# Kernel optimization log

Measured on AMD Instinct MI355X. Metric: run time of the kernel, lower is better.

## Reference

```python
import jax, jax.numpy as jnp
import numpy as np

N = 100000       # nodes
E = 1000000      # edges
IN = 128         # in_dim
HID = 64         # hid_dim
NET = 4          # n_etypes
STEPS = 5        # n_steps
G = 128          # graphs in batch
LBL = 10         # num_labels


def setup_inputs() -> dict:
    key = jax.random.key(0)
    ks = jax.random.split(key, 20)
    def w(k, shape, fan_in):
        return jax.random.normal(k, shape, jnp.float32) / np.sqrt(fan_in)
    return dict(
        x=jax.random.normal(ks[0], (N, IN), jnp.float32),
        src=jax.random.randint(ks[1], (E,), 0, N),
        dst=jax.random.randint(ks[2], (E,), 0, N),
        etype=jax.random.randint(ks[3], (E,), 0, NET),
        node2graph=jnp.sort(jax.random.randint(ks[4], (N,), 0, G)),
        # linear_in
        W_in=w(ks[5], (HID, IN), IN), b_in=jnp.zeros((HID,), jnp.float32),
        # per-edge-type linears [n_etypes, out, in]
        We=w(ks[6], (NET, HID, HID), HID), be=jnp.zeros((NET, HID), jnp.float32),
        # GRUCell (torch layout: rows = [r; z; n])
        W_ih=w(ks[7], (3 * HID, HID), HID), b_ih=jnp.zeros((3 * HID,), jnp.float32),
        W_hh=w(ks[8], (3 * HID, HID), HID), b_hh=jnp.zeros((3 * HID,), jnp.float32),
        # classifier
        W1=w(ks[9], (HID // 2, HID), HID), b1=jnp.zeros((HID // 2,), jnp.float32),
        W2=w(ks[10], (LBL, HID // 2), HID // 2), b2=jnp.zeros((LBL,), jnp.float32),
    )


def reference(x, W_in, b_in, We, be, W_ih, b_ih, W_hh, b_hh, W1, b1, W2, b2,
              src, dst, etype, node2graph):
    h = x @ W_in.T + b_in                                  # [N, HID]
    for _ in range(STEPS):
        # per-etype linear on node states: trans[e] = h @ We[e].T + be[e]
        trans = jnp.einsum('nd,efd->enf', h, We) + be[:, None, :]  # [NET, N, HID]
        msgs = trans[etype, src]                           # [E, HID] gather per edge
        a = jax.ops.segment_sum(msgs, dst, num_segments=N)  # scatter-add aggregation
        # GRUCell(a, h)
        gi = a @ W_ih.T + b_ih
        gh = h @ W_hh.T + b_hh
        ir, iz, i_n = jnp.split(gi, 3, axis=-1)
        hr, hz, h_n = jnp.split(gh, 3, axis=-1)
        r = jax.nn.sigmoid(ir + hr)
        z = jax.nn.sigmoid(iz + hz)
        n = jnp.tanh(i_n + r * h_n)
        h = (1.0 - z) * n + z * h
    # dgl.mean_nodes: per-graph mean of node states
    cnt = jnp.maximum(jax.ops.segment_sum(jnp.ones((N,), h.dtype), node2graph, num_segments=G), 1.0)
    hg = jax.ops.segment_sum(h, node2graph, num_segments=G) / cnt[:, None]  # [G, HID]
    return jax.nn.relu(hg @ W1.T + b1) @ W2.T + b2         # [G, LBL]
```

## Files before the change

kernel.cpp:

```cpp
#include <hip/hip_runtime.h>
#include <hip/hip_bf16.h>
#include <math.h>

#define N_NODES 100000
#define N_EDGES 1000000
#define IN_DIM 128
#define HID 64
#define NET 4
#define STEPS 5
#define G_GRAPHS 128
#define LBL 10
#define NGRP 6250
#define NBKT 1024
#define TILE_E 8192

typedef __attribute__((ext_vector_type(8))) short short8;
typedef __attribute__((ext_vector_type(4))) float f32x4;
typedef unsigned short ushort_t;

__device__ inline ushort_t f2bf(float v) {
    __hip_bfloat16 b = __float2bfloat16(v);
    return __builtin_bit_cast(ushort_t, b);
}
__device__ inline float bf2f(ushort_t u) {
    __hip_bfloat16 b = __builtin_bit_cast(__hip_bfloat16, u);
    return __bfloat162float(b);
}


__global__ void k_pack_bc(const float* __restrict__ We, ushort_t* __restrict__ BC) {
    int idx = blockIdx.x * blockDim.x + threadIdx.x;
    if (idx >= 24 * 4 * 64 * 8) return;
    int j = idx & 7, lane = (idx >> 3) & 63, ct = (idx >> 9) & 3, sl = idx >> 11;
    int g = lane >> 4, u = lane & 15;
    int p = sl >> 3, ks = sl & 7;
    int k = ks * 32 + g * 8 + j;
    int t = k >> 6, d = k & 63;
    int o = ct * 16 + u;
    float val = We[t * 4096 + o * 64 + d];
    ushort_t hi = f2bf(val);
    BC[idx] = (p < 2) ? hi : f2bf(val - bf2f(hi));
}

__global__ void k_pack_b2(const float* __restrict__ W_ih, const float* __restrict__ b_ih,
                          const float* __restrict__ W_hh, const float* __restrict__ b_hh,
                          ushort_t* __restrict__ B2, float* __restrict__ bg2) {
    int idx = blockIdx.x * blockDim.x + threadIdx.x;
    if (idx >= 12 * 16 * 4 * 16 * 8) return;
    int j = idx & 7, u = (idx >> 3) & 15, g = (idx >> 7) & 3, ct = (idx >> 9) & 15, s = idx >> 13;
    int m = ct * 16 + u;
    int q = m >> 6, gate = (m >> 4) & 3, c = q * 16 + (m & 15);
    int k = (s & 3) * 32 + g * 8 + j;
    float val;
    if (gate == 0)      { int jr = c;        val = (k < 64) ? W_ih[jr * 64 + k] : W_hh[jr * 64 + k - 64]; }
    else if (gate == 1) { int jr = 64 + c;   val = (k < 64) ? W_ih[jr * 64 + k] : W_hh[jr * 64 + k - 64]; }
    else if (gate == 2) { int jr = 128 + c;  val = (k < 64) ? W_ih[jr * 64 + k] : 0.f; }
    else                { int jr = 128 + c;  val = (k < 64) ? 0.f : W_hh[jr * 64 + k - 64]; }
    ushort_t hi = f2bf(val);
    B2[idx] = (s < 8) ? hi : f2bf(val - bf2f(hi));
    if (s == 0 && g == 0 && j == 0) {
        float bv;
        if (gate == 0)      bv = b_ih[c] + b_hh[c];
        else if (gate == 1) bv = b_ih[64 + c] + b_hh[64 + c];
        else if (gate == 2) bv = b_ih[128 + c];
        else                bv = b_hh[128 + c];
        bg2[m] = bv;
    }
}

__global__ void k_pack_bin(const float* __restrict__ W_in, ushort_t* __restrict__ BIN) {
    int idx = blockIdx.x * blockDim.x + threadIdx.x;
    if (idx >= 24576) return;
    int j = idx & 7, lu = (idx >> 3) & 63, ct = (idx >> 9) & 3, s = idx >> 11;
    int g = lu >> 4, u = lu & 15;
    int m = ct * 16 + u;
    int k = (s & 3) * 32 + g * 8 + j;
    float val = W_in[m * 128 + k];
    ushort_t hi = f2bf(val);
    BIN[idx] = (s < 8) ? hi : f2bf(val - bf2f(hi));
}

__global__ __launch_bounds__(256) void k_linear_in(const float* __restrict__ x,
        const ushort_t* __restrict__ BIN, const float* __restrict__ b_in,
        ushort_t* __restrict__ hrow, ushort_t* __restrict__ lrow) {
    __shared__ float hlds[4][16 * 68];
    int tid = threadIdx.x;
    int lane = tid & 63, wp = tid >> 6;
    int g = lane >> 4, u = lane & 15;
    int grp = blockIdx.x * 4 + wp;
    bool ok = grp < NGRP;
    int row = ok ? (grp * 16 + u) : 0;
    short8 xhi[4], xlo[4];
    #pragma unroll
    for (int ks = 0; ks < 4; ++ks) {
        const float* xp = &x[(size_t)row * 128 + ks * 32 + g * 8];
        float4 v0 = ok ? *(const float4*)xp : make_float4(0.f, 0.f, 0.f, 0.f);
        float4 v1 = ok ? *(const float4*)(xp + 4) : make_float4(0.f, 0.f, 0.f, 0.f);
        float vv[8] = {v0.x, v0.y, v0.z, v0.w, v1.x, v1.y, v1.z, v1.w};
        #pragma unroll
        for (int j = 0; j < 8; ++j) {
            ushort_t hh = f2bf(vv[j]);
            xhi[ks][j] = (short)hh;
            xlo[ks][j] = (short)f2bf(vv[j] - bf2f(hh));
        }
    }
    f32x4 zero = {0.f, 0.f, 0.f, 0.f};
    f32x4 acc[4] = {zero, zero, zero, zero};
    #pragma unroll
    for (int s = 0; s < 12; ++s) {
        int ks = s & 3;
        short8 af = (s < 4) ? xhi[ks] : (s < 8) ? xlo[ks] : xhi[ks];
        #pragma unroll
        for (int ct = 0; ct < 4; ++ct) {
            short8 bf = *(const short8*)&BIN[((size_t)(s * 4 + ct) * 64 + lane) * 8];
            acc[ct] = __builtin_amdgcn_mfma_f32_16x16x32_bf16(af, bf, acc[ct], 0, 0, 0);
        }
    }
    #pragma unroll
    for (int ct = 0; ct < 4; ++ct) {
        float bo = b_in[ct * 16 + u];
        #pragma unroll
        for (int j = 0; j < 4; ++j)
            hlds[wp][(g * 4 + j) * 68 + ct * 16 + u] = acc[ct][j] + bo;
    }
    __syncthreads();
    #pragma unroll
    for (int k = 0; k < 4; ++k) {
        int bi = g + 4 * k;
        short8 ov;
        #pragma unroll
        for (int j = 0; j < 8; ++j) {
            float v = hlds[wp][u * 68 + (bi & 7) * 8 + j];
            ushort_t hh = f2bf(v);
            ov[j] = (bi < 8) ? (short)hh : (short)f2bf(v - bf2f(hh));
        }
        if (ok) {
            size_t base = (size_t)(grp * 16 + u) * 64;
            if (bi < 8) *(short8*)&hrow[base + bi * 8] = ov;
            else        *(short8*)&lrow[base + (bi - 8) * 8] = ov;
        }
    }
}

__global__ __launch_bounds__(256) void k_bhist(const int* __restrict__ dst,
        int* __restrict__ bhist) {
    __shared__ int h[NBKT];
    for (int i = threadIdx.x; i < NBKT; i += 256) h[i] = 0;
    __syncthreads();
    int idx = blockIdx.x * 256 + threadIdx.x;
    for (int e = idx; e < N_EDGES; e += 256 * 256) atomicAdd(&h[dst[e] >> 7], 1);
    __syncthreads();
    for (int i = threadIdx.x; i < NBKT; i += 256) {
        int c = h[i];
        if (c) atomicAdd(&bhist[i], c);
    }
}

__global__ __launch_bounds__(1024) void k_bscan(const int* __restrict__ bhist,
        int* __restrict__ bbase, int* __restrict__ bcursor) {
    __shared__ int ts[NBKT];
    int t = threadIdx.x;
    int v = bhist[t];
    ts[t] = v;
    __syncthreads();
    for (int off = 1; off < NBKT; off <<= 1) {
        int u = (t >= off) ? ts[t - off] : 0;
        __syncthreads();
        ts[t] += u;
        __syncthreads();
    }
    int excl = ts[t] - v;
    bbase[t] = excl;
    bcursor[t] = excl;
    if (t == NBKT - 1) bbase[NBKT] = ts[NBKT - 1];
}

__global__ __launch_bounds__(512) void k_bscatter(const int* __restrict__ src,
        const int* __restrict__ dst, const int* __restrict__ et,
        int* __restrict__ bcursor, unsigned int* __restrict__ ebuf) {
    __shared__ int hcnt[NBKT], loff[NBKT], gpos[NBKT], ps[512];
    __shared__ unsigned int stage[TILE_E];
    __shared__ unsigned short sbkt[TILE_E];
    int tid = threadIdx.x;
    int base = blockIdx.x * TILE_E;
    int tilecnt = min(TILE_E, N_EDGES - base);
    for (int i = tid; i < NBKT; i += 512) hcnt[i] = 0;
    __syncthreads();
    #pragma unroll
    for (int k = 0; k < TILE_E / 512; ++k) {
        int e = base + tid + k * 512;
        if (e < N_EDGES) atomicAdd(&hcnt[dst[e] >> 7], 1);
    }
    __syncthreads();
    int c0 = hcnt[tid * 2], c1 = hcnt[tid * 2 + 1];
    ps[tid] = c0 + c1;
    __syncthreads();
    for (int off = 1; off < 512; off <<= 1) {
        int u = (tid >= off) ? ps[tid - off] : 0;
        __syncthreads();
        ps[tid] += u;
        __syncthreads();
    }
    int ex = ps[tid] - (c0 + c1);
    loff[tid * 2] = ex;
    loff[tid * 2 + 1] = ex + c0;
    for (int b = tid; b < NBKT; b += 512) {
        int c = hcnt[b];
        gpos[b] = c ? atomicAdd(&bcursor[b], c) : 0;
    }
    __syncthreads();
    for (int i = tid; i < NBKT; i += 512) hcnt[i] = 0;
    __syncthreads();
    #pragma unroll
    for (int k = 0; k < TILE_E / 512; ++k) {
        int e = base + tid + k * 512;
        if (e < N_EDGES) {
            int d = dst[e];
            int b = d >> 7;
            int r = atomicAdd(&hcnt[b], 1);
            int lp = loff[b] + r;
            stage[lp] = (unsigned int)src[e] | ((unsigned int)et[e] << 20)
                      | ((unsigned int)(d & 127) << 22);
            sbkt[lp] = (unsigned short)b;
        }
    }
    __syncthreads();
    for (int i = tid; i < tilecnt; i += 512) {
        int b = sbkt[i];
        ebuf[gpos[b] + (i - loff[b])] = stage[i];
    }
}

__global__ __launch_bounds__(256) void k_bcsr(const unsigned int* __restrict__ ebuf,
        const int* __restrict__ bbase, int* __restrict__ adj, int* __restrict__ row_ptr2) {
    __shared__ int ncnt[512], noff[513], ps[256];
    int b = blockIdx.x;
    int tid = threadIdx.x;
    int ebeg = bbase[b], eend = bbase[b + 1];
    int ecnt = eend - ebeg;
    ncnt[tid] = 0; ncnt[tid + 256] = 0;
    __syncthreads();
    for (int i = tid; i < ecnt; i += 256) {
        unsigned int p = ebuf[ebeg + i];
        int key = (int)((((p >> 22) & 127) << 2) | ((p >> 20) & 3));
        atomicAdd(&ncnt[key], 1);
    }
    __syncthreads();
    int c0 = ncnt[2 * tid], c1 = ncnt[2 * tid + 1];
    ps[tid] = c0 + c1;
    __syncthreads();
    for (int off = 1; off < 256; off <<= 1) {
        int u = (tid >= off) ? ps[tid - off] : 0;
        __syncthreads();
        ps[tid] += u;
        __syncthreads();
    }
    int ex = ps[tid] - (c0 + c1);
    noff[2 * tid] = ex;
    noff[2 * tid + 1] = ex + c0;
    if (tid == 255) noff[512] = ps[255];
    __syncthreads();
    ncnt[tid] = 0; ncnt[tid + 256] = 0;
    __syncthreads();
    for (int i = tid; i < ecnt; i += 256) {
        unsigned int p = ebuf[ebeg + i];
        int key = (int)((((p >> 22) & 127) << 2) | ((p >> 20) & 3));
        int r = atomicAdd(&ncnt[key], 1);
        adj[ebeg + noff[key] + r] = (int)(p & 0xFFFFF);
    }
    for (int k = tid; k < 512; k += 256)
        row_ptr2[b * 512 + k] = ebeg + noff[k];
    if (b == NBKT - 1 && tid == 0) row_ptr2[NBKT * 512] = eend;
}

__global__ __launch_bounds__(512) void k_step(const int* __restrict__ row_ptr2,
        const int* __restrict__ adj, const ushort_t* __restrict__ hin,
        const ushort_t* __restrict__ lin, ushort_t* __restrict__ hout,
        ushort_t* __restrict__ lout,
        const ushort_t* __restrict__ BC, const float* __restrict__ be,
        const ushort_t* __restrict__ B2, const float* __restrict__ bg2) {
    __shared__ float smem[8448];
    float* aggf = smem;
    float* cnts = smem + 8320;
    ushort_t* als  = (ushort_t*)smem;
    ushort_t* hlds = (ushort_t*)((char*)smem + 9216);

    int tid = threadIdx.x, lane = tid & 63, wp = tid >> 6;
    int g = lane >> 4, u = lane & 15;
    int grp0 = blockIdx.x * 2;
    int nbase = grp0 * 16;

    #pragma unroll 1
    for (int pr = 0; pr < 2; ++pr) {
        int nl0 = wp * 4 + pr * 2;
        const int* op = &row_ptr2[(size_t)(nbase + nl0) * 4];
        int b0 = op[0], b1 = op[1], b2 = op[2], b3 = op[3], b4 = op[4];
        int b5 = op[5], b6 = op[6], b7 = op[7], b8 = op[8];
        int i0 = b0, i1 = b1, i2 = b2, i3 = b3, i4 = b4, i5 = b5, i6 = b6, i7 = b7;
        float s0 = 0.f, s1 = 0.f, s2 = 0.f, s3 = 0.f, s4 = 0.f, s5 = 0.f, s6 = 0.f, s7 = 0.f;
        bool c0 = i0 < b1, c1 = i1 < b2, c2 = i2 < b3, c3 = i3 < b4;
        bool c4 = i4 < b5, c5 = i5 < b6, c6 = i6 < b7, c7 = i7 < b8;
        int a0 = adj[c0 ? i0 : 0], a1 = adj[c1 ? i1 : 0];
        int a2 = adj[c2 ? i2 : 0], a3 = adj[c3 ? i3 : 0];
        int a4 = adj[c4 ? i4 : 0], a5 = adj[c5 ? i5 : 0];
        int a6 = adj[c6 ? i6 : 0], a7 = adj[c7 ? i7 : 0];
        while (c0 | c1 | c2 | c3 | c4 | c5 | c6 | c7) {
            ushort_t w0 = hin[(size_t)a0 * 64 + lane];
            ushort_t w1 = hin[(size_t)a1 * 64 + lane];
            ushort_t w2 = hin[(size_t)a2 * 64 + lane];
            ushort_t w3 = hin[(size_t)a3 * 64 + lane];
            ushort_t w4 = hin[(size_t)a4 * 64 + lane];
            ushort_t w5 = hin[(size_t)a5 * 64 + lane];
            ushort_t w6 = hin[(size_t)a6 * 64 + lane];
            ushort_t w7 = hin[(size_t)a7 * 64 + lane];
            i0 += c0; i1 += c1; i2 += c2; i3 += c3;
            i4 += c4; i5 += c5; i6 += c6; i7 += c7;
            s0 += c0 ? bf2f(w0) : 0.f;
            s1 += c1 ? bf2f(w1) : 0.f;
            s2 += c2 ? bf2f(w2) : 0.f;
            s3 += c3 ? bf2f(w3) : 0.f;
            s4 += c4 ? bf2f(w4) : 0.f;
            s5 += c5 ? bf2f(w5) : 0.f;
            s6 += c6 ? bf2f(w6) : 0.f;
            s7 += c7 ? bf2f(w7) : 0.f;
            c0 = i0 < b1; c1 = i1 < b2; c2 = i2 < b3; c3 = i3 < b4;
            c4 = i4 < b5; c5 = i5 < b6; c6 = i6 < b7; c7 = i7 < b8;
            a0 = adj[c0 ? i0 : 0]; a1 = adj[c1 ? i1 : 0];
            a2 = adj[c2 ? i2 : 0]; a3 = adj[c3 ? i3 : 0];
            a4 = adj[c4 ? i4 : 0]; a5 = adj[c5 ? i5 : 0];
            a6 = adj[c6 ? i6 : 0]; a7 = adj[c7 ? i7 : 0];
        }
        aggf[nl0 * 260 +   0 + lane] = s0;
        aggf[nl0 * 260 +  64 + lane] = s1;
        aggf[nl0 * 260 + 128 + lane] = s2;
        aggf[nl0 * 260 + 192 + lane] = s3;
        aggf[(nl0 + 1) * 260 +   0 + lane] = s4;
        aggf[(nl0 + 1) * 260 +  64 + lane] = s5;
        aggf[(nl0 + 1) * 260 + 128 + lane] = s6;
        aggf[(nl0 + 1) * 260 + 192 + lane] = s7;
        if (lane == 0) {
            cnts[nl0 * 4 + 0] = (float)(b1 - b0);
            cnts[nl0 * 4 + 1] = (float)(b2 - b1);
            cnts[nl0 * 4 + 2] = (float)(b3 - b2);
            cnts[nl0 * 4 + 3] = (float)(b4 - b3);
            cnts[(nl0 + 1) * 4 + 0] = (float)(b5 - b4);
            cnts[(nl0 + 1) * 4 + 1] = (float)(b6 - b5);
            cnts[(nl0 + 1) * 4 + 2] = (float)(b7 - b6);
            cnts[(nl0 + 1) * 4 + 3] = (float)(b8 - b7);
        }
    }
    __syncthreads();

    int rp1 = wp >> 2, cq = wp & 3;
    f32x4 zero = {0.f, 0.f, 0.f, 0.f};
    f32x4 acc1 = zero;
    #pragma unroll
    for (int ks = 0; ks < 8; ++ks) {
        const float* ap = &aggf[(rp1 * 16 + u) * 260 + ks * 32 + g * 8];
        f32x4 x0 = *(const f32x4*)ap;
        f32x4 x1 = *(const f32x4*)(ap + 4);
        short8 ahi, alo;
        #pragma unroll
        for (int j = 0; j < 4; ++j) {
            ushort_t hh = f2bf(x0[j]);
            ahi[j] = (short)hh; alo[j] = (short)f2bf(x0[j] - bf2f(hh));
            ushort_t hh2 = f2bf(x1[j]);
            ahi[4 + j] = (short)hh2; alo[4 + j] = (short)f2bf(x1[j] - bf2f(hh2));
        }
        #pragma unroll
        for (int p = 0; p < 3; ++p) {
            short8 af = (p == 1) ? alo : ahi;
            short8 bf = *(const short8*)&BC[((size_t)((p * 8 + ks) * 4 + cq) * 64 + lane) * 8];
            acc1 = __builtin_amdgcn_mfma_f32_16x16x32_bf16(af, bf, acc1, 0, 0, 0);
        }
    }
    __syncthreads();

    {
        float beL[4];
        #pragma unroll
        for (int t = 0; t < 4; ++t) beL[t] = be[t * 64 + cq * 16 + u];
        #pragma unroll
        for (int j = 0; j < 4; ++j) {
            int row = rp1 * 16 + g * 4 + j;
            f32x4 cn = *(const f32x4*)&cnts[row * 4];
            float v = acc1[j] + cn[0] * beL[0] + cn[1] * beL[1]
                              + cn[2] * beL[2] + cn[3] * beL[3];
            int col = cq * 16 + u;
            ushort_t hh = f2bf(v);
            als[row * 136 + col] = hh;
            als[row * 136 + 64 + col] = f2bf(v - bf2f(hh));
        }
    }
    {
        int c = tid;
        int gl = c >> 8, rr = c & 255, bi = rr >> 4, uu = rr & 15;
        size_t base = (size_t)(nbase + gl * 16 + uu) * 64;
        short8 v = (bi < 8) ? *(const short8*)&hin[base + bi * 8]
                            : *(const short8*)&lin[base + (bi - 8) * 8];
        *(short8*)&hlds[((gl * 16 + bi) * 16 + uu) * 8] = v;
    }
    __syncthreads();

    int q = wp & 3, rp2 = wp >> 2;
    f32x4 acc2[4] = {zero, zero, zero, zero};
    #pragma unroll
    for (int s = 0; s < 12; ++s) {
        int p2 = s >> 2, ks2 = s & 3;
        short8 afr;
        if (ks2 < 2) {
            int base = ((p2 == 1) ? 64 : 0) + ks2 * 32 + g * 8;
            afr = *(const short8*)&als[(rp2 * 16 + u) * 136 + base];
        } else {
            int part = (p2 == 1) ? 1 : 0;
            int bi = part * 8 + (ks2 - 2) * 4 + g;
            afr = *(const short8*)&hlds[((rp2 * 16 + bi) * 16 + u) * 8];
        }
        #pragma unroll
        for (int ct = 0; ct < 4; ++ct) {
            short8 bfr = *(const short8*)&B2[((size_t)(s * 16 + q * 4 + ct) * 64 + g * 16 + u) * 8];
            acc2[ct] = __builtin_amdgcn_mfma_f32_16x16x32_bf16(afr, bfr, acc2[ct], 0, 0, 0);
        }
    }
    __syncthreads();

    {
        float bgv[4];
        #pragma unroll
        for (int ct = 0; ct < 4; ++ct) bgv[ct] = bg2[q * 64 + ct * 16 + u];
        int hid = q * 16 + u;
        #pragma unroll
        for (int j = 0; j < 4; ++j) {
            int uu = g * 4 + j;
            int shi = ((rp2 * 16 + (hid >> 3)) * 16 + uu) * 8 + (hid & 7);
            int slo = ((rp2 * 16 + 8 + (hid >> 3)) * 16 + uu) * 8 + (hid & 7);
            float ho = bf2f(hlds[shi]) + bf2f(hlds[slo]);
            float rs  = acc2[0][j] + bgv[0];
            float zs  = acc2[1][j] + bgv[1];
            float inn = acc2[2][j] + bgv[2];
            float hnn = acc2[3][j] + bgv[3];
            float rr = 1.f / (1.f + __expf(-rs));
            float zz = 1.f / (1.f + __expf(-zs));
            float t = inn + rr * hnn;
            float e2 = __expf(2.f * t);
            float nn = 1.f - 2.f / (e2 + 1.f);
            float hnew = (1.f - zz) * nn + zz * ho;
            ushort_t hh = f2bf(hnew);
            hlds[shi] = hh;
            hlds[slo] = f2bf(hnew - bf2f(hh));
        }
    }
    __syncthreads();

    {
        int c = tid;
        int gl = c >> 8, rr = c & 255, bi = rr >> 4, uu = rr & 15;
        short8 v = *(const short8*)&hlds[((gl * 16 + bi) * 16 + uu) * 8];
        size_t base = (size_t)(nbase + gl * 16 + uu) * 64;
        if (bi < 8) *(short8*)&hout[base + bi * 8] = v;
        else        *(short8*)&lout[base + (bi - 8) * 8] = v;
    }
}

__global__ __launch_bounds__(256) void k_pool(const int* __restrict__ n2g,
        const ushort_t* __restrict__ hrow, const ushort_t* __restrict__ lrow,
        float* __restrict__ hg) {
    int gidx = blockIdx.x;
    int lo = 0, hi = N_NODES;
    while (lo < hi) { int mid = (lo + hi) >> 1; if (n2g[mid] < gidx) lo = mid + 1; else hi = mid; }
    int s = lo;
    hi = N_NODES;
    while (lo < hi) { int mid = (lo + hi) >> 1; if (n2g[mid] < gidx + 1) lo = mid + 1; else hi = mid; }
    int e = lo;
    int w = threadIdx.x >> 6, lane = threadIdx.x & 63;
    float sum = 0.f;
    for (int n = s + w; n < e; n += 4)
        sum += bf2f(hrow[(size_t)n * 64 + lane]) + bf2f(lrow[(size_t)n * 64 + lane]);
    __shared__ float red[4][64];
    red[w][lane] = sum;
    __syncthreads();
    if (threadIdx.x < 64) {
        float tot = red[0][lane] + red[1][lane] + red[2][lane] + red[3][lane];
        float cnt = (float)(e - s);
        hg[gidx * 64 + lane] = tot / fmaxf(cnt, 1.f);
    }
}

__global__ __launch_bounds__(64) void k_cls(const float* __restrict__ hg,
        const float* __restrict__ W1, const float* __restrict__ b1,
        const float* __restrict__ W2, const float* __restrict__ b2,
        float* __restrict__ out) {
    int gidx = blockIdx.x;
    __shared__ float v[64];
    __shared__ float m[32];
    v[threadIdx.x] = hg[gidx * 64 + threadIdx.x];
    __syncthreads();
    if (threadIdx.x < 32) {
        float a = b1[threadIdx.x];
        #pragma unroll 8
        for (int k = 0; k < 64; ++k) a = fmaf(v[k], W1[threadIdx.x * 64 + k], a);
        m[threadIdx.x] = fmaxf(a, 0.f);
    }
    __syncthreads();
    if (threadIdx.x < 10) {
        float a = b2[threadIdx.x];
        #pragma unroll
        for (int j = 0; j < 32; ++j) a = fmaf(m[j], W2[threadIdx.x * 32 + j], a);
        out[gidx * 10 + threadIdx.x] = a;
    }
}

extern "C" void kernel_launch(void* const* d_in, const int* in_sizes, int n_in,
                              void* d_out, int out_size, void* d_ws, size_t ws_size,
                              hipStream_t stream) {
    const float* x    = (const float*)d_in[0];
    const int* src    = (const int*)d_in[1];
    const int* dst    = (const int*)d_in[2];
    const int* etype  = (const int*)d_in[3];
    const int* n2g    = (const int*)d_in[4];
    const float* W_in = (const float*)d_in[5];
    const float* b_in = (const float*)d_in[6];
    const float* We   = (const float*)d_in[7];
    const float* be   = (const float*)d_in[8];
    const float* W_ih = (const float*)d_in[9];
    const float* b_ih = (const float*)d_in[10];
    const float* W_hh = (const float*)d_in[11];
    const float* b_hh = (const float*)d_in[12];
    const float* W1   = (const float*)d_in[13];
    const float* b1   = (const float*)d_in[14];
    const float* W2   = (const float*)d_in[15];
    const float* b2   = (const float*)d_in[16];
    float* out = (float*)d_out;

    char* wsb = (char*)d_ws;
    size_t off = 0;
    auto alloc = [&](size_t bytes) -> void* {
        void* p = wsb + off;
        off += (bytes + 255) & ~(size_t)255;
        return p;
    };
    ushort_t* hrowA    = (ushort_t*)alloc((size_t)N_NODES * 64 * 2);
    ushort_t* lrowA    = (ushort_t*)alloc((size_t)N_NODES * 64 * 2);
    ushort_t* hrowB    = (ushort_t*)alloc((size_t)N_NODES * 64 * 2);
    ushort_t* lrowB    = (ushort_t*)alloc((size_t)N_NODES * 64 * 2);
    int*      adj      = (int*)     alloc((size_t)N_EDGES * 4);
    unsigned int* ebuf = (unsigned int*)alloc((size_t)N_EDGES * 4);
    int*      row_ptr2 = (int*)     alloc(((size_t)NBKT * 512 + 1) * 4);
    int*      bhist    = (int*)     alloc((size_t)NBKT * 4);
    int*      bbase    = (int*)     alloc((size_t)(NBKT + 1) * 4);
    int*      bcursor  = (int*)     alloc((size_t)NBKT * 4);
    ushort_t* B2       = (ushort_t*)alloc((size_t)12 * 16 * 4 * 16 * 8 * 2);
    float*    bg2      = (float*)   alloc(256 * 4);
    ushort_t* BIN      = (ushort_t*)alloc((size_t)24576 * 2);
    ushort_t* BC       = (ushort_t*)alloc((size_t)24 * 4 * 64 * 8 * 2);
    float*    hg       = (float*)   alloc(128 * 64 * 4);

    hipLaunchKernelGGL(k_pack_b2, dim3(384), dim3(256), 0, stream, W_ih, b_ih, W_hh, b_hh, B2, bg2);
    hipLaunchKernelGGL(k_pack_bin, dim3(96), dim3(256), 0, stream, W_in, BIN);
    hipLaunchKernelGGL(k_pack_bc, dim3(192), dim3(256), 0, stream, We, BC);
    hipLaunchKernelGGL(k_linear_in, dim3((NGRP + 3) / 4), dim3(256), 0, stream, x, BIN, b_in, hrowA, lrowA);

    hipMemsetAsync(bhist, 0, (size_t)NBKT * 4, stream);
    hipLaunchKernelGGL(k_bhist, dim3(256), dim3(256), 0, stream, dst, bhist);
    hipLaunchKernelGGL(k_bscan, dim3(1), dim3(1024), 0, stream, bhist, bbase, bcursor);
    hipLaunchKernelGGL(k_bscatter, dim3((N_EDGES + TILE_E - 1) / TILE_E), dim3(512), 0, stream,
                       src, dst, etype, bcursor, ebuf);
    hipLaunchKernelGGL(k_bcsr, dim3(NBKT), dim3(256), 0, stream, ebuf, bbase, adj, row_ptr2);

    int sblk = NGRP / 2;
    for (int step = 0; step < STEPS; ++step) {
        const ushort_t* hin = (step & 1) ? hrowB : hrowA;
        const ushort_t* lin = (step & 1) ? lrowB : lrowA;
        ushort_t* hout      = (step & 1) ? hrowA : hrowB;
        ushort_t* lout      = (step & 1) ? lrowA : lrowB;
        hipLaunchKernelGGL(k_step, dim3(sblk), dim3(512), 0, stream,
                           row_ptr2, adj, hin, lin, hout, lout, BC, be, B2, bg2);
    }
    hipLaunchKernelGGL(k_pool, dim3(G_GRAPHS), dim3(256), 0, stream, n2g, hrowB, lrowB, hg);
    hipLaunchKernelGGL(k_cls, dim3(G_GRAPHS), dim3(64), 0, stream, hg, W1, b1, W2, b2, out);
}
```

Baseline: 816.7 us.

## Balance per-block edge aggregation across waves with LDS atomics; truncate bf16 splits

The per-node, per-etype segmented gather loop is replaced. Each wave now takes an equal slice of the block's contiguous edge range and accumulates into LDS with float atomics, using node and etype bits packed into the adjacency word. This targets load imbalance and the idle lanes of the old eight-way predicated loop, at the cost of LDS atomic contention and an extra zeroing pass. Separately, the bf16 hi/lo splits now use bit truncation instead of round-to-nearest conversion, which saves some ALU work and keeps the hi+lo split accurate.

```diff
diff --git a/kernel.cpp b/kernel.cpp
--- a/kernel.cpp
+++ b/kernel.cpp
@@ -232,7 +232,8 @@
 }
 
 __global__ __launch_bounds__(256) void k_bcsr(const unsigned int* __restrict__ ebuf,
-        const int* __restrict__ bbase, int* __restrict__ adj, int* __restrict__ row_ptr2) {
+        const int* __restrict__ bbase, unsigned int* __restrict__ adj,
+        int* __restrict__ row_ptr2) {
     __shared__ int ncnt[512], noff[513], ps[256];
     int b = blockIdx.x;
     int tid = threadIdx.x;
@@ -266,7 +267,7 @@
         unsigned int p = ebuf[ebeg + i];
         int key = (int)((((p >> 22) & 127) << 2) | ((p >> 20) & 3));
         int r = atomicAdd(&ncnt[key], 1);
-        adj[ebeg + noff[key] + r] = (int)(p & 0xFFFFF);
+        adj[ebeg + noff[key] + r] = p & 0x07FFFFFFu;
     }
     for (int k = tid; k < 512; k += 256)
         row_ptr2[b * 512 + k] = ebeg + noff[k];
@@ -274,14 +275,14 @@
 }
 
 __global__ __launch_bounds__(512) void k_step(const int* __restrict__ row_ptr2,
-        const int* __restrict__ adj, const ushort_t* __restrict__ hin,
+        const unsigned int* __restrict__ adj, const ushort_t* __restrict__ hin,
         const ushort_t* __restrict__ lin, ushort_t* __restrict__ hout,
         ushort_t* __restrict__ lout,
         const ushort_t* __restrict__ BC, const float* __restrict__ be,
         const ushort_t* __restrict__ B2, const float* __restrict__ bg2) {
     __shared__ float smem[8448];
+    __shared__ int rp[129];
     float* aggf = smem;
-    float* cnts = smem + 8320;
     ushort_t* als  = (ushort_t*)smem;
     ushort_t* hlds = (ushort_t*)((char*)smem + 9216);
 
@@ -290,63 +291,44 @@
     int grp0 = blockIdx.x * 2;
     int nbase = grp0 * 16;
 
-    #pragma unroll 1
-    for (int pr = 0; pr < 2; ++pr) {
-        int nl0 = wp * 4 + pr * 2;
-        const int* op = &row_ptr2[(size_t)(nbase + nl0) * 4];
-        int b0 = op[0], b1 = op[1], b2 = op[2], b3 = op[3], b4 = op[4];
-        int b5 = op[5], b6 = op[6], b7 = op[7], b8 = op[8];
-        int i0 = b0, i1 = b1, i2 = b2, i3 = b3, i4 = b4, i5 = b5, i6 = b6, i7 = b7;
-        float s0 = 0.f, s1 = 0.f, s2 = 0.f, s3 = 0.f, s4 = 0.f, s5 = 0.f, s6 = 0.f, s7 = 0.f;
-        bool c0 = i0 < b1, c1 = i1 < b2, c2 = i2 < b3, c3 = i3 < b4;
-        bool c4 = i4 < b5, c5 = i5 < b6, c6 = i6 < b7, c7 = i7 < b8;
-        int a0 = adj[c0 ? i0 : 0], a1 = adj[c1 ? i1 : 0];
-        int a2 = adj[c2 ? i2 : 0], a3 = adj[c3 ? i3 : 0];
-        int a4 = adj[c4 ? i4 : 0], a5 = adj[c5 ? i5 : 0];
-        int a6 = adj[c6 ? i6 : 0], a7 = adj[c7 ? i7 : 0];
-        while (c0 | c1 | c2 | c3 | c4 | c5 | c6 | c7) {
-            ushort_t w0 = hin[(size_t)a0 * 64 + lane];
-            ushort_t w1 = hin[(size_t)a1 * 64 + lane];
-            ushort_t w2 = hin[(size_t)a2 * 64 + lane];
-            ushort_t w3 = hin[(size_t)a3 * 64 + lane];
-            ushort_t w4 = hin[(size_t)a4 * 64 + lane];
-            ushort_t w5 = hin[(size_t)a5 * 64 + lane];
-            ushort_t w6 = hin[(size_t)a6 * 64 + lane];
-            ushort_t w7 = hin[(size_t)a7 * 64 + lane];
-            i0 += c0; i1 += c1; i2 += c2; i3 += c3;
-            i4 += c4; i5 += c5; i6 += c6; i7 += c7;
-            s0 += c0 ? bf2f(w0) : 0.f;
-            s1 += c1 ? bf2f(w1) : 0.f;
-            s2 += c2 ? bf2f(w2) : 0.f;
-            s3 += c3 ? bf2f(w3) : 0.f;
-            s4 += c4 ? bf2f(w4) : 0.f;
-            s5 += c5 ? bf2f(w5) : 0.f;
-            s6 += c6 ? bf2f(w6) : 0.f;
-            s7 += c7 ? bf2f(w7) : 0.f;
-            c0 = i0 < b1; c1 = i1 < b2; c2 = i2 < b3; c3 = i3 < b4;
-            c4 = i4 < b5; c5 = i5 < b6; c6 = i6 < b7; c7 = i7 < b8;
-            a0 = adj[c0 ? i0 : 0]; a1 = adj[c1 ? i1 : 0];
-            a2 = adj[c2 ? i2 : 0]; a3 = adj[c3 ? i3 : 0];
-            a4 = adj[c4 ? i4 : 0]; a5 = adj[c5 ? i5 : 0];
-            a6 = adj[c6 ? i6 : 0]; a7 = adj[c7 ? i7 : 0];
-        }
-        aggf[nl0 * 260 +   0 + lane] = s0;
-        aggf[nl0 * 260 +  64 + lane] = s1;
-        aggf[nl0 * 260 + 128 + lane] = s2;
-        aggf[nl0 * 260 + 192 + lane] = s3;
-        aggf[(nl0 + 1) * 260 +   0 + lane] = s4;
-        aggf[(nl0 + 1) * 260 +  64 + lane] = s5;
-        aggf[(nl0 + 1) * 260 + 128 + lane] = s6;
-        aggf[(nl0 + 1) * 260 + 192 + lane] = s7;
-        if (lane == 0) {
-            cnts[nl0 * 4 + 0] = (float)(b1 - b0);
-            cnts[nl0 * 4 + 1] = (float)(b2 - b1);
-            cnts[nl0 * 4 + 2] = (float)(b3 - b2);
-            cnts[nl0 * 4 + 3] = (float)(b4 - b3);
-            cnts[(nl0 + 1) * 4 + 0] = (float)(b5 - b4);
-            cnts[(nl0 + 1) * 4 + 1] = (float)(b6 - b5);
-            cnts[(nl0 + 1) * 4 + 2] = (float)(b7 - b6);
-            cnts[(nl0 + 1) * 4 + 3] = (float)(b8 - b7);
+    #pragma unroll
+    for (int i = 0; i < 17; ++i) {
+        int idx = i * 512 + tid;
+        if (idx < 8320) aggf[idx] = 0.f;
+    }
+    if (tid < 129) rp[tid] = row_ptr2[nbase * 4 + tid];
+    __syncthreads();
+
+    {
+        int E0 = rp[0], E1 = rp[128];
+        int per = (E1 - E0 + 7) >> 3;
+        int e0 = E0 + wp * per;
+        int e1 = min(e0 + per, E1);
+        int e = e0;
+        for (; e + 8 <= e1; e += 8) {
+            unsigned p0 = adj[e],     p1 = adj[e + 1], p2 = adj[e + 2], p3 = adj[e + 3];
+            unsigned p4 = adj[e + 4], p5 = adj[e + 5], p6 = adj[e + 6], p7 = adj[e + 7];
+            float v0 = bf2f(hin[(p0 & 0xFFFFFu) * 64u + (unsigned)lane]);
+            float v1 = bf2f(hin[(p1 & 0xFFFFFu) * 64u + (unsigned)lane]);
+            float v2 = bf2f(hin[(p2 & 0xFFFFFu) * 64u + (unsigned)lane]);
+            float v3 = bf2f(hin[(p3 & 0xFFFFFu) * 64u + (unsigned)lane]);
+            float v4 = bf2f(hin[(p4 & 0xFFFFFu) * 64u + (unsigned)lane]);
+            float v5 = bf2f(hin[(p5 & 0xFFFFFu) * 64u + (unsigned)lane]);
+            float v6 = bf2f(hin[(p6 & 0xFFFFFu) * 64u + (unsigned)lane]);
+            float v7 = bf2f(hin[(p7 & 0xFFFFFu) * 64u + (unsigned)lane]);
+            atomicAdd(&aggf[((p0 >> 22) & 31) * 260 + ((p0 >> 20) & 3) * 64 + lane], v0);
+            atomicAdd(&aggf[((p1 >> 22) & 31) * 260 + ((p1 >> 20) & 3) * 64 + lane], v1);
+            atomicAdd(&aggf[((p2 >> 22) & 31) * 260 + ((p2 >> 20) & 3) * 64 + lane], v2);
+            atomicAdd(&aggf[((p3 >> 22) & 31) * 260 + ((p3 >> 20) & 3) * 64 + lane], v3);
+            atomicAdd(&aggf[((p4 >> 22) & 31) * 260 + ((p4 >> 20) & 3) * 64 + lane], v4);
+            atomicAdd(&aggf[((p5 >> 22) & 31) * 260 + ((p5 >> 20) & 3) * 64 + lane], v5);
+            atomicAdd(&aggf[((p6 >> 22) & 31) * 260 + ((p6 >> 20) & 3) * 64 + lane], v6);
+            atomicAdd(&aggf[((p7 >> 22) & 31) * 260 + ((p7 >> 20) & 3) * 64 + lane], v7);
+        }
+        for (; e < e1; ++e) {
+            unsigned p = adj[e];
+            float v = bf2f(hin[(p & 0xFFFFFu) * 64u + (unsigned)lane]);
+            atomicAdd(&aggf[((p >> 22) & 31) * 260 + ((p >> 20) & 3) * 64 + lane], v);
         }
     }
     __syncthreads();
@@ -362,10 +344,14 @@
         short8 ahi, alo;
         #pragma unroll
         for (int j = 0; j < 4; ++j) {
-            ushort_t hh = f2bf(x0[j]);
-            ahi[j] = (short)hh; alo[j] = (short)f2bf(x0[j] - bf2f(hh));
-            ushort_t hh2 = f2bf(x1[j]);
-            ahi[4 + j] = (short)hh2; alo[4 + j] = (short)f2bf(x1[j] - bf2f(hh2));
+            unsigned b0 = __builtin_bit_cast(unsigned, x0[j]);
+            ahi[j] = (short)(b0 >> 16);
+            float l0 = x0[j] - __builtin_bit_cast(float, b0 & 0xFFFF0000u);
+            alo[j] = (short)(__builtin_bit_cast(unsigned, l0) >> 16);
+            unsigned b1 = __builtin_bit_cast(unsigned, x1[j]);
+            ahi[4 + j] = (short)(b1 >> 16);
+            float l1 = x1[j] - __builtin_bit_cast(float, b1 & 0xFFFF0000u);
+            alo[4 + j] = (short)(__builtin_bit_cast(unsigned, l1) >> 16);
         }
         #pragma unroll
         for (int p = 0; p < 3; ++p) {
@@ -383,13 +369,16 @@
         #pragma unroll
         for (int j = 0; j < 4; ++j) {
             int row = rp1 * 16 + g * 4 + j;
-            f32x4 cn = *(const f32x4*)&cnts[row * 4];
-            float v = acc1[j] + cn[0] * beL[0] + cn[1] * beL[1]
-                              + cn[2] * beL[2] + cn[3] * beL[3];
+            float c0 = (float)(rp[row * 4 + 1] - rp[row * 4 + 0]);
+            float c1 = (float)(rp[row * 4 + 2] - rp[row * 4 + 1]);
+            float c2 = (float)(rp[row * 4 + 3] - rp[row * 4 + 2]);
+            float c3 = (float)(rp[row * 4 + 4] - rp[row * 4 + 3]);
+            float v = acc1[j] + c0 * beL[0] + c1 * beL[1] + c2 * beL[2] + c3 * beL[3];
             int col = cq * 16 + u;
-            ushort_t hh = f2bf(v);
-            als[row * 136 + col] = hh;
-            als[row * 136 + 64 + col] = f2bf(v - bf2f(hh));
+            unsigned bv = __builtin_bit_cast(unsigned, v);
+            als[row * 136 + col] = (ushort_t)(bv >> 16);
+            float lo = v - __builtin_bit_cast(float, bv & 0xFFFF0000u);
+            als[row * 136 + 64 + col] = (ushort_t)(__builtin_bit_cast(unsigned, lo) >> 16);
         }
     }
     {
@@ -445,9 +434,10 @@
             float e2 = __expf(2.f * t);
             float nn = 1.f - 2.f / (e2 + 1.f);
             float hnew = (1.f - zz) * nn + zz * ho;
-            ushort_t hh = f2bf(hnew);
-            hlds[shi] = hh;
-            hlds[slo] = f2bf(hnew - bf2f(hh));
+            unsigned hb = __builtin_bit_cast(unsigned, hnew);
+            hlds[shi] = (ushort_t)(hb >> 16);
+            float lo2 = hnew - __builtin_bit_cast(float, hb & 0xFFFF0000u);
+            hlds[slo] = (ushort_t)(__builtin_bit_cast(unsigned, lo2) >> 16);
         }
     }
     __syncthreads();
@@ -543,7 +533,7 @@
     ushort_t* lrowA    = (ushort_t*)alloc((size_t)N_NODES * 64 * 2);
     ushort_t* hrowB    = (ushort_t*)alloc((size_t)N_NODES * 64 * 2);
     ushort_t* lrowB    = (ushort_t*)alloc((size_t)N_NODES * 64 * 2);
-    int*      adj      = (int*)     alloc((size_t)N_EDGES * 4);
+    unsigned int* adj  = (unsigned int*)alloc((size_t)N_EDGES * 4);
     unsigned int* ebuf = (unsigned int*)alloc((size_t)N_EDGES * 4);
     int*      row_ptr2 = (int*)     alloc(((size_t)NBKT * 512 + 1) * 4);
     int*      bhist    = (int*)     alloc((size_t)NBKT * 4);
```

Result: slower. 1.992 ms (+143.9%).
